# Optimization experiments

Hardware: AMD Instinct MI355X
Metric: run time of the kernel (lower is better)

## Reference

```python
import jax, jax.numpy as jnp
import numpy as np

SEG = 24      # segment_size
NH = 8        # n_heads
THETA = 10000.0


def setup_inputs() -> dict:
    key = jax.random.key(0)
    ks = jax.random.split(key, 6)
    B, T, H, W, D = 8, 96, 32, 32, 64
    in_dim = SEG * D          # 1536
    hid_dim = (SEG // 2) * D  # 768
    n_seg = T // SEG          # 4
    x = jax.random.normal(ks[0], (B, T, H, W, D), dtype=jnp.float32)
    # rotary frequencies: freqs_cis[t, j] = exp(i * t * theta^{-2j/hid_dim})
    inv = 1.0 / (THETA ** (np.arange(0, hid_dim, 2, dtype=np.float32) / hid_dim))
    ang = np.arange(n_seg, dtype=np.float32)[:, None] * inv[None, :]  # (n, hid/2)
    freqs_cos = jnp.asarray(np.cos(ang), dtype=jnp.float32)
    freqs_sin = jnp.asarray(np.sin(ang), dtype=jnp.float32)
    s = 0.02
    Wq = jax.random.normal(ks[1], (in_dim, hid_dim), dtype=jnp.float32) * s
    Wk = jax.random.normal(ks[2], (in_dim, hid_dim), dtype=jnp.float32) * s
    Wv = jax.random.normal(ks[3], (in_dim, hid_dim), dtype=jnp.float32) * s
    Wo = jax.random.normal(ks[4], (hid_dim, in_dim), dtype=jnp.float32) * s
    bo = jnp.zeros((in_dim,), dtype=jnp.float32)
    return {"x": x, "freqs_cos": freqs_cos, "freqs_sin": freqs_sin,
            "Wq": Wq, "Wk": Wk, "Wv": Wv, "Wo": Wo, "bo": bo}


def _rope(q, cos, sin):
    # q: (b, n, hid); pairs (even, odd) rotated by complex multiply
    q2 = q.reshape(*q.shape[:-1], -1, 2)
    qr = q2[..., 0] * cos - q2[..., 1] * sin
    qi = q2[..., 0] * sin + q2[..., 1] * cos
    return jnp.stack([qr, qi], axis=-1).reshape(q.shape)


def reference(x, freqs_cos, freqs_sin, Wq, Wk, Wv, Wo, bo):
    B, T, H, W, D = x.shape
    n = T // SEG
    hid = Wq.shape[1]
    hd = hid // NH
    # (b t h w d) -> ((b h w) n (p d)) ; T divisible by SEG so no padding
    xr = jnp.transpose(x, (0, 2, 3, 1, 4)).reshape(B * H * W, T, D)
    xs = xr.reshape(B * H * W, n, SEG * D)
    q = jnp.einsum('bne,eh->bnh', xs, Wq)
    k = jnp.einsum('bne,eh->bnh', xs, Wk)
    v = jnp.einsum('bne,eh->bnh', xs, Wv)
    cos, sin = freqs_cos[:n][None], freqs_sin[:n][None]  # (1, n, hid/2)
    q = _rope(q, cos, sin)
    k = _rope(k, cos, sin)
    # split heads: b n (h d) -> b h n d
    def heads(t):
        return jnp.transpose(t.reshape(B * H * W, n, NH, hd), (0, 2, 1, 3))
    qh, kh, vh = heads(q), heads(k), heads(v)
    scores = jnp.einsum('bhnd,bhmd->bhnm', qh, kh) / jnp.sqrt(jnp.float32(hd))
    attn = jax.nn.softmax(scores, axis=-1)
    o = jnp.einsum('bhnm,bhmd->bhnd', attn, vh)
    o = jnp.transpose(o, (0, 2, 1, 3)).reshape(B * H * W, n, hid)
    o = jnp.einsum('bnh,he->bne', o, Wo) + bo
    # b n (p d) -> b (n p) d -> (B,T,H,W,D)
    o = o.reshape(B * H * W, T, D)
    o = o.reshape(B, H, W, T, D)
    return jnp.transpose(o, (0, 3, 1, 2, 4))
```

## Files before the change

### kernel.cpp

```cpp
#include <hip/hip_runtime.h>
#include <hip/hip_bf16.h>

using bf16 = __hip_bfloat16;
using short8 = __attribute__((ext_vector_type(8))) short;
using floatx4 = __attribute__((ext_vector_type(4))) float;

#define NSEG 4
#define HID 768
#define INDIM 1536
#define NQKV 2304
#define NHEADS 8
#define HD 96

__device__ inline unsigned short f2b(float v) {
  union { float f; unsigned u; } c; c.f = v;
  unsigned r = c.u + 0x7FFF + ((c.u >> 16) & 1);
  return (unsigned short)(r >> 16);
}
__device__ inline float b2f(unsigned short u) {
  union { unsigned v; float f; } c; c.v = ((unsigned)u) << 16; return c.f;
}

__device__ inline void gload16(const void* g, void* l) {
  __builtin_amdgcn_global_load_lds(
      (const __attribute__((address_space(1))) unsigned int*)g,
      (__attribute__((address_space(3))) unsigned int*)l, 16, 0, 0);
}

#define MEMFENCE asm volatile("" ::: "memory")
#define BARRIER do { MEMFENCE; __builtin_amdgcn_s_barrier(); MEMFENCE; } while (0)

#define PHASE(par, q, LOADB, STAGES, VMW) do {                                 \
    short8 a00 = *(const short8*)(lA + (par)*65536 + (q)*2048);                \
    short8 a01 = *(const short8*)(lA + (par)*65536 + (q)*2048 + 16384);        \
    short8 a10 = *(const short8*)(lA + (par)*65536 + (q)*2048 + 1024);         \
    short8 a11 = *(const short8*)(lA + (par)*65536 + (q)*2048 + 1024 + 16384); \
    if (LOADB) {                                                               \
      _Pragma("unroll")                                                        \
      for (int fn = 0; fn < 4; ++fn) {                                         \
        bfr[fn][0] = *(const short8*)(lB + (par)*65536 + fn*1024);             \
        bfr[fn][1] = *(const short8*)(lB + (par)*65536 + fn*1024 + 16384);     \
      }                                                                        \
    }                                                                          \
    STAGES;                                                                    \
    BARRIER;                                                                   \
    __builtin_amdgcn_s_setprio(1);                                             \
    _Pragma("unroll")                                                          \
    for (int fn = 0; fn < 4; ++fn) {                                           \
      acc[2*(q)][fn]   = __builtin_amdgcn_mfma_f32_16x16x32_bf16(              \
          a00, bfr[fn][0], acc[2*(q)][fn], 0, 0, 0);                           \
      acc[2*(q)][fn]   = __builtin_amdgcn_mfma_f32_16x16x32_bf16(              \
          a01, bfr[fn][1], acc[2*(q)][fn], 0, 0, 0);                           \
      acc[2*(q)+1][fn] = __builtin_amdgcn_mfma_f32_16x16x32_bf16(              \
          a10, bfr[fn][0], acc[2*(q)+1][fn], 0, 0, 0);                         \
      acc[2*(q)+1][fn] = __builtin_amdgcn_mfma_f32_16x16x32_bf16(              \
          a11, bfr[fn][1], acc[2*(q)+1][fn], 0, 0, 0);                         \
    }                                                                          \
    __builtin_amdgcn_s_setprio(0);                                             \
    VMW;                                                                       \
    BARRIER;                                                                   \
  } while (0)

#define VM4 do { asm volatile("s_waitcnt vmcnt(4)" ::: "memory"); } while (0)
#define VM0 do { asm volatile("s_waitcnt vmcnt(0)" ::: "memory"); } while (0)

__global__ __launch_bounds__(256) void transpose_w(
    const float* __restrict__ src, bf16* __restrict__ dst, int K, int C) {
  __shared__ unsigned short tile[32][33];
  const int c0 = blockIdx.x * 32, k0 = blockIdx.y * 32;
  const int tx = threadIdx.x, ty = threadIdx.y;
#pragma unroll
  for (int i = 0; i < 4; ++i)
    tile[ty + 8 * i][tx] = f2b(src[(size_t)(k0 + ty + 8 * i) * C + c0 + tx]);
  __syncthreads();
  unsigned short* d = (unsigned short*)dst;
#pragma unroll
  for (int i = 0; i < 4; ++i)
    d[(size_t)(c0 + ty + 8 * i) * K + k0 + tx] = tile[tx][ty + 8 * i];
}

__global__ __launch_bounds__(256) void transpose_w3(
    const float* __restrict__ s0, const float* __restrict__ s1,
    const float* __restrict__ s2, bf16* __restrict__ dst) {
  __shared__ unsigned short tile[32][33];
  const float* srcs[3] = {s0, s1, s2};
  const float* src = srcs[blockIdx.z];
  bf16* dz = dst + (size_t)blockIdx.z * HID * INDIM;
  const int c0 = blockIdx.x * 32, k0 = blockIdx.y * 32;
  const int tx = threadIdx.x, ty = threadIdx.y;
#pragma unroll
  for (int i = 0; i < 4; ++i)
    tile[ty + 8 * i][tx] = f2b(src[(size_t)(k0 + ty + 8 * i) * HID + c0 + tx]);
  __syncthreads();
  unsigned short* d = (unsigned short*)dz;
#pragma unroll
  for (int i = 0; i < 4; ++i)
    d[(size_t)(c0 + ty + 8 * i) * INDIM + k0 + tx] = tile[tx][ty + 8 * i];
}

__global__ __launch_bounds__(256) void convert_x(
    const float* __restrict__ x, bf16* __restrict__ xb) {
  const size_t i = ((size_t)blockIdx.x * 256 + threadIdx.x) * 8;
  float4 a = *(const float4*)(x + i);
  float4 b = *(const float4*)(x + i + 4);
  union { uint4 u; unsigned short s[8]; } r;
  r.s[0] = f2b(a.x); r.s[1] = f2b(a.y); r.s[2] = f2b(a.z); r.s[3] = f2b(a.w);
  r.s[4] = f2b(b.x); r.s[5] = f2b(b.y); r.s[6] = f2b(b.z); r.s[7] = f2b(b.w);
  *(uint4*)(xb + i) = r.u;
}

__global__ __launch_bounds__(512, 2) void gemm_qkv(
    const bf16* __restrict__ xb, const bf16* __restrict__ wT,
    bf16* __restrict__ qkv) {
  __shared__ __align__(16) char lds[131072];
  const int tid = threadIdx.x;
  const int lane = tid & 63, wave = tid >> 6;
  const int wr = wave >> 2, wc = wave & 3;
  const int l15 = lane & 15, quad = lane >> 4;

  const int lt = (blockIdx.x & 7) * 144 + (blockIdx.x >> 3);
  const int n0 = (lt % 9) * 256;
  const int m0 = (lt / 9) * 256;

  const int srow = wave * 16 + (lane >> 2);
  const int dswz = ((lane & 3) * 8) ^ ((lane & 32) >> 1);
  const bf16* asrc[2];
  const bf16* bsrc[2];
#pragma unroll
  for (int h = 0; h < 2; ++h) {
    const int m = m0 + h * 128 + srow;
    const int r = m >> 2, n = m & 3;
    const int b = r >> 10, hw = r & 1023;
    asrc[h] = xb + ((size_t)((b * 96 + n * 24) * 1024 + hw)) * 64 + dswz;
    bsrc[h] = wT + (size_t)(n0 + h * 128 + srow) * INDIM + dswz;
  }
  char* sdst = lds + wave * 1024;

#define STAGE_QA(kt, h) do {                                   \
    char* d_ = sdst + (((kt) & 1) * 65536) + (h) * 8192;       \
    const bf16* s_ = asrc[h] + (size_t)(kt) * 65536;           \
    gload16(s_, d_);                                           \
    gload16(s_ + 32, d_ + 16384);                              \
  } while (0)
#define STAGE_QB(kt, h) do {                                   \
    char* d_ = sdst + 32768 + (((kt) & 1) * 65536) + (h) * 8192; \
    const bf16* s_ = bsrc[h] + (size_t)(kt) * 64;              \
    gload16(s_, d_);                                           \
    gload16(s_ + 32, d_ + 16384);                              \
  } while (0)

  const int lofs = l15 * 64 + ((quad * 16) ^ ((l15 & 8) << 2));
  const char* lA = lds + wr * 8192 + lofs;
  const char* lB = lds + 32768 + wc * 4096 + lofs;

  floatx4 acc[8][4] = {};
  short8 bfr[4][2];

  STAGE_QB(0, 0); STAGE_QB(0, 1); STAGE_QA(0, 0); STAGE_QA(0, 1);
  STAGE_QB(1, 0); STAGE_QB(1, 1);
  VM4;
  BARRIER;

  const int NKT = 24;
  for (int i = 0; i < 12; ++i) {
    const int a = 2 * i;
    PHASE(0, 0, 1, { STAGE_QA(a + 1, 0); }, {});
    PHASE(0, 1, 0, { STAGE_QA(a + 1, 1); }, {});
    PHASE(0, 2, 0, { if (a + 2 < NKT) STAGE_QB(a + 2, 0); }, {});
    PHASE(0, 3, 0, { if (a + 2 < NKT) STAGE_QB(a + 2, 1); },
          { if (a + 2 < NKT) VM4; else VM0; });
    PHASE(1, 0, 1, { if (a + 2 < NKT) STAGE_QA(a + 2, 0); }, {});
    PHASE(1, 1, 0, { if (a + 2 < NKT) STAGE_QA(a + 2, 1); }, {});
    PHASE(1, 2, 0, { if (a + 3 < NKT) STAGE_QB(a + 3, 0); }, {});
    PHASE(1, 3, 0, { if (a + 3 < NKT) STAGE_QB(a + 3, 1); },
          { if (a + 3 < NKT) VM4; else VM0; });
  }
#undef STAGE_QA
#undef STAGE_QB

#pragma unroll
  for (int fm = 0; fm < 8; ++fm)
#pragma unroll
    for (int fn = 0; fn < 4; ++fn)
#pragma unroll
      for (int reg = 0; reg < 4; ++reg) {
        const int row = m0 + wr * 128 + fm * 16 + quad * 4 + reg;
        const int col = n0 + wc * 64 + fn * 16 + l15;
        qkv[(size_t)row * NQKV + col] = __float2bfloat16(acc[fm][fn][reg]);
      }
}

__global__ __launch_bounds__(256) void attn_kernel(
    const bf16* __restrict__ qkv, const float* __restrict__ fcos,
    const float* __restrict__ fsin, bf16* __restrict__ obuf) {
  const int wave = threadIdx.x >> 6, lane = threadIdx.x & 63;
  const int r = blockIdx.x * 4 + wave;
  const int c0 = lane * 12;
  const int j0 = lane * 6;
  const bf16* base = qkv + (size_t)r * (NSEG * NQKV) + c0;

  float q[NSEG][12], k[NSEG][12];
#pragma unroll
  for (int n = 0; n < NSEG; ++n) {
    const bf16* row = base + (size_t)n * NQKV;
    union { uint2 u[3]; unsigned short s[12]; } Q, K;
#pragma unroll
    for (int t = 0; t < 3; ++t) {
      Q.u[t] = *(const uint2*)(row + 4 * t);
      K.u[t] = *(const uint2*)(row + HID + 4 * t);
    }
    const float* cp = fcos + n * (HID / 2) + j0;
    const float* sp = fsin + n * (HID / 2) + j0;
#pragma unroll
    for (int t = 0; t < 6; ++t) {
      const float cc = cp[t], ss = sp[t];
      const float a = b2f(Q.s[2 * t]), b = b2f(Q.s[2 * t + 1]);
      q[n][2 * t] = a * cc - b * ss;
      q[n][2 * t + 1] = a * ss + b * cc;
      const float e = b2f(K.s[2 * t]), f = b2f(K.s[2 * t + 1]);
      k[n][2 * t] = e * cc - f * ss;
      k[n][2 * t + 1] = e * ss + f * cc;
    }
  }

  float P[NSEG][NSEG];
#pragma unroll
  for (int n = 0; n < NSEG; ++n)
#pragma unroll
    for (int m = 0; m < NSEG; ++m) {
      float s = 0.f;
#pragma unroll
      for (int t = 0; t < 12; ++t) s += q[n][t] * k[m][t];
      s += __shfl_xor(s, 1, 64);
      s += __shfl_xor(s, 2, 64);
      s += __shfl_xor(s, 4, 64);
      P[n][m] = s * 0.10206207261596575f;
    }
#pragma unroll
  for (int n = 0; n < NSEG; ++n) {
    const float mx = fmaxf(fmaxf(P[n][0], P[n][1]), fmaxf(P[n][2], P[n][3]));
    float sum = 0.f;
#pragma unroll
    for (int m = 0; m < NSEG; ++m) {
      P[n][m] = __expf(P[n][m] - mx);
      sum += P[n][m];
    }
    const float inv = 1.f / sum;
#pragma unroll
    for (int m = 0; m < NSEG; ++m) P[n][m] *= inv;
  }

  float v[NSEG][12];
#pragma unroll
  for (int n = 0; n < NSEG; ++n) {
    union { uint2 u[3]; unsigned short s[12]; } V;
#pragma unroll
    for (int t = 0; t < 3; ++t)
      V.u[t] = *(const uint2*)(base + (size_t)n * NQKV + 2 * HID + 4 * t);
#pragma unroll
    for (int t = 0; t < 12; ++t) v[n][t] = b2f(V.s[t]);
  }
  bf16* orow = obuf + (size_t)r * (NSEG * HID) + c0;
#pragma unroll
  for (int n = 0; n < NSEG; ++n) {
    union { uint2 u[3]; unsigned w[6]; } O;
#pragma unroll
    for (int t = 0; t < 6; ++t) {
      float o0 = 0.f, o1 = 0.f;
#pragma unroll
      for (int m = 0; m < NSEG; ++m) {
        o0 += P[n][m] * v[m][2 * t];
        o1 += P[n][m] * v[m][2 * t + 1];
      }
      O.w[t] = (unsigned)f2b(o0) | ((unsigned)f2b(o1) << 16);
    }
#pragma unroll
    for (int t = 0; t < 3; ++t)
      *(uint2*)(orow + (size_t)n * HID + 4 * t) = O.u[t];
  }
}

__global__ __launch_bounds__(512, 2) void gemm_out(
    const bf16* __restrict__ Ao, const bf16* __restrict__ wT,
    const float* __restrict__ bo, float* __restrict__ out) {
  __shared__ __align__(16) char lds[131072];
  const int tid = threadIdx.x;
  const int lane = tid & 63, wave = tid >> 6;
  const int wr = wave >> 2, wc = wave & 3;
  const int l15 = lane & 15, quad = lane >> 4;

  const int lt = (blockIdx.x & 7) * 96 + (blockIdx.x >> 3);
  const int n0 = (lt % 6) * 256;
  const int m0 = (lt / 6) * 256;

  const int srow = wave * 16 + (lane >> 2);
  const int dswz = ((lane & 3) * 8) ^ ((lane & 32) >> 1);
  const bf16* asrc[2];
  const bf16* bsrc[2];
#pragma unroll
  for (int h = 0; h < 2; ++h) {
    asrc[h] = Ao + (size_t)(m0 + h * 128 + srow) * HID + dswz;
    bsrc[h] = wT + (size_t)(n0 + h * 128 + srow) * HID + dswz;
  }
  char* sdst = lds + wave * 1024;

#define STAGE_OA(kt, h) do {                                   \
    char* d_ = sdst + (((kt) & 1) * 65536) + (h) * 8192;       \
    const bf16* s_ = asrc[h] + (size_t)(kt) * 64;              \
    gload16(s_, d_);                                           \
    gload16(s_ + 32, d_ + 16384);                              \
  } while (0)
#define STAGE_OB(kt, h) do {                                   \
    char* d_ = sdst + 32768 + (((kt) & 1) * 65536) + (h) * 8192; \
    const bf16* s_ = bsrc[h] + (size_t)(kt) * 64;              \
    gload16(s_, d_);                                           \
    gload16(s_ + 32, d_ + 16384);                              \
  } while (0)

  const int lofs = l15 * 64 + ((quad * 16) ^ ((l15 & 8) << 2));
  const char* lA = lds + wr * 8192 + lofs;
  const char* lB = lds + 32768 + wc * 4096 + lofs;

  floatx4 acc[8][4] = {};
  short8 bfr[4][2];

  STAGE_OB(0, 0); STAGE_OB(0, 1); STAGE_OA(0, 0); STAGE_OA(0, 1);
  STAGE_OB(1, 0); STAGE_OB(1, 1);
  VM4;
  BARRIER;

  const int NKT = 12;
  for (int i = 0; i < 6; ++i) {
    const int a = 2 * i;
    PHASE(0, 0, 1, { STAGE_OA(a + 1, 0); }, {});
    PHASE(0, 1, 0, { STAGE_OA(a + 1, 1); }, {});
    PHASE(0, 2, 0, { if (a + 2 < NKT) STAGE_OB(a + 2, 0); }, {});
    PHASE(0, 3, 0, { if (a + 2 < NKT) STAGE_OB(a + 2, 1); },
          { if (a + 2 < NKT) VM4; else VM0; });
    PHASE(1, 0, 1, { if (a + 2 < NKT) STAGE_OA(a + 2, 0); }, {});
    PHASE(1, 1, 0, { if (a + 2 < NKT) STAGE_OA(a + 2, 1); }, {});
    PHASE(1, 2, 0, { if (a + 3 < NKT) STAGE_OB(a + 3, 0); }, {});
    PHASE(1, 3, 0, { if (a + 3 < NKT) STAGE_OB(a + 3, 1); },
          { if (a + 3 < NKT) VM4; else VM0; });
  }
#undef STAGE_OA
#undef STAGE_OB

#pragma unroll
  for (int fm = 0; fm < 8; ++fm)
#pragma unroll
    for (int fn = 0; fn < 4; ++fn)
#pragma unroll
      for (int reg = 0; reg < 4; ++reg) {
        const int row = m0 + wr * 128 + fm * 16 + quad * 4 + reg;
        const int col = n0 + wc * 64 + fn * 16 + l15;
        const float v = acc[fm][fn][reg] + bo[col];
        const int r = row >> 2, n = row & 3;
        const int b = r >> 10, hw = r & 1023;
        const int p = col >> 6, d = col & 63;
        const size_t dst =
            ((size_t)((b * 96 + n * 24 + p) * 1024 + hw)) * 64 + d;
        out[dst] = v;
      }
}

extern "C" void kernel_launch(void* const* d_in, const int* in_sizes, int n_in,
                              void* d_out, int out_size, void* d_ws,
                              size_t ws_size, hipStream_t stream) {
  const float* x = (const float*)d_in[0];
  const float* fcos = (const float*)d_in[1];
  const float* fsin = (const float*)d_in[2];
  const float* Wq = (const float*)d_in[3];
  const float* Wk = (const float*)d_in[4];
  const float* Wv = (const float*)d_in[5];
  const float* Wo = (const float*)d_in[6];
  const float* bo = (const float*)d_in[7];
  float* out = (float*)d_out;

  char* ws = (char*)d_ws;
  bf16* wqkvT = (bf16*)ws;
  bf16* woT = (bf16*)(ws + 7077888);
  bf16* qkv = (bf16*)(ws + 9437184);
  bf16* obuf = (bf16*)(ws + 160432128);
  bf16* xb = (bf16*)d_out;

  dim3 tb(32, 8);
  transpose_w3<<<dim3(24, 48, 3), tb, 0, stream>>>(Wq, Wk, Wv, wqkvT);
  transpose_w<<<dim3(48, 24), tb, 0, stream>>>(Wo, woT, HID, INDIM);

  convert_x<<<24576, 256, 0, stream>>>(x, xb);
  gemm_qkv<<<1152, 512, 0, stream>>>(xb, wqkvT, qkv);
  attn_kernel<<<2048, 256, 0, stream>>>(qkv, fcos, fsin, obuf);
  gemm_out<<<768, 512, 0, stream>>>(obuf, woT, bo, out);
}
```

Baseline: 684.3 us.

## Merge weight transposes into one launch, widen convert_x, restructure attention Q loading

Combines the two weight-transpose kernels into one launch over a 48x48x4 grid, with an early exit for out-of-range tiles, to save a launch. convert_x now handles 16 elements per thread with half as many blocks. The attention kernel loads and rotates Q one segment at a time inside the score loop instead of keeping all Q in registers, and adds an occupancy hint of 4 blocks via launch bounds, to lower register pressure. The merged grid launches idle blocks for the smaller Wo shape.

```diff
diff --git a/kernel.cpp b/kernel.cpp
--- a/kernel.cpp
+++ b/kernel.cpp
@@ -64,49 +64,48 @@
 #define VM4 do { asm volatile("s_waitcnt vmcnt(4)" ::: "memory"); } while (0)
 #define VM0 do { asm volatile("s_waitcnt vmcnt(0)" ::: "memory"); } while (0)
 
-__global__ __launch_bounds__(256) void transpose_w(
-    const float* __restrict__ src, bf16* __restrict__ dst, int K, int C) {
+__global__ __launch_bounds__(256) void transpose_all(
+    const float* __restrict__ Wq, const float* __restrict__ Wk,
+    const float* __restrict__ Wv, const float* __restrict__ Wo,
+    bf16* __restrict__ wqkvT, bf16* __restrict__ woT) {
   __shared__ unsigned short tile[32][33];
+  const int z = blockIdx.z;
+  const float* src;
+  unsigned short* dst;
+  int K, C;
+  if (z < 3) {
+    src = (z == 0) ? Wq : (z == 1) ? Wk : Wv;
+    dst = (unsigned short*)(wqkvT + (size_t)z * HID * INDIM);
+    K = INDIM; C = HID;
+  } else {
+    src = Wo;
+    dst = (unsigned short*)woT;
+    K = HID; C = INDIM;
+  }
   const int c0 = blockIdx.x * 32, k0 = blockIdx.y * 32;
+  if (c0 >= C || k0 >= K) return;
   const int tx = threadIdx.x, ty = threadIdx.y;
 #pragma unroll
   for (int i = 0; i < 4; ++i)
     tile[ty + 8 * i][tx] = f2b(src[(size_t)(k0 + ty + 8 * i) * C + c0 + tx]);
   __syncthreads();
-  unsigned short* d = (unsigned short*)dst;
 #pragma unroll
   for (int i = 0; i < 4; ++i)
-    d[(size_t)(c0 + ty + 8 * i) * K + k0 + tx] = tile[tx][ty + 8 * i];
-}
-
-__global__ __launch_bounds__(256) void transpose_w3(
-    const float* __restrict__ s0, const float* __restrict__ s1,
-    const float* __restrict__ s2, bf16* __restrict__ dst) {
-  __shared__ unsigned short tile[32][33];
-  const float* srcs[3] = {s0, s1, s2};
-  const float* src = srcs[blockIdx.z];
-  bf16* dz = dst + (size_t)blockIdx.z * HID * INDIM;
-  const int c0 = blockIdx.x * 32, k0 = blockIdx.y * 32;
-  const int tx = threadIdx.x, ty = threadIdx.y;
-#pragma unroll
-  for (int i = 0; i < 4; ++i)
-    tile[ty + 8 * i][tx] = f2b(src[(size_t)(k0 + ty + 8 * i) * HID + c0 + tx]);
-  __syncthreads();
-  unsigned short* d = (unsigned short*)dz;
-#pragma unroll
-  for (int i = 0; i < 4; ++i)
-    d[(size_t)(c0 + ty + 8 * i) * INDIM + k0 + tx] = tile[tx][ty + 8 * i];
+    dst[(size_t)(c0 + ty + 8 * i) * K + k0 + tx] = tile[tx][ty + 8 * i];
 }
 
 __global__ __launch_bounds__(256) void convert_x(
     const float* __restrict__ x, bf16* __restrict__ xb) {
-  const size_t i = ((size_t)blockIdx.x * 256 + threadIdx.x) * 8;
-  float4 a = *(const float4*)(x + i);
-  float4 b = *(const float4*)(x + i + 4);
-  union { uint4 u; unsigned short s[8]; } r;
-  r.s[0] = f2b(a.x); r.s[1] = f2b(a.y); r.s[2] = f2b(a.z); r.s[3] = f2b(a.w);
-  r.s[4] = f2b(b.x); r.s[5] = f2b(b.y); r.s[6] = f2b(b.z); r.s[7] = f2b(b.w);
-  *(uint4*)(xb + i) = r.u;
+  const size_t i = ((size_t)blockIdx.x * 256 + threadIdx.x) * 16;
+#pragma unroll
+  for (int h = 0; h < 2; ++h) {
+    float4 a = *(const float4*)(x + i + 8 * h);
+    float4 b = *(const float4*)(x + i + 8 * h + 4);
+    union { uint4 u; unsigned short s[8]; } r;
+    r.s[0] = f2b(a.x); r.s[1] = f2b(a.y); r.s[2] = f2b(a.z); r.s[3] = f2b(a.w);
+    r.s[4] = f2b(b.x); r.s[5] = f2b(b.y); r.s[6] = f2b(b.z); r.s[7] = f2b(b.w);
+    *(uint4*)(xb + i + 8 * h) = r.u;
+  }
 }
 
 __global__ __launch_bounds__(512, 2) void gemm_qkv(
@@ -190,7 +189,7 @@
       }
 }
 
-__global__ __launch_bounds__(256) void attn_kernel(
+__global__ __launch_bounds__(256, 4) void attn_kernel(
     const bf16* __restrict__ qkv, const float* __restrict__ fcos,
     const float* __restrict__ fsin, bf16* __restrict__ obuf) {
   const int wave = threadIdx.x >> 6, lane = threadIdx.x & 63;
@@ -199,24 +198,18 @@
   const int j0 = lane * 6;
   const bf16* base = qkv + (size_t)r * (NSEG * NQKV) + c0;
 
-  float q[NSEG][12], k[NSEG][12];
+  float k[NSEG][12];
 #pragma unroll
   for (int n = 0; n < NSEG; ++n) {
-    const bf16* row = base + (size_t)n * NQKV;
-    union { uint2 u[3]; unsigned short s[12]; } Q, K;
-#pragma unroll
-    for (int t = 0; t < 3; ++t) {
-      Q.u[t] = *(const uint2*)(row + 4 * t);
-      K.u[t] = *(const uint2*)(row + HID + 4 * t);
-    }
+    union { uint2 u[3]; unsigned short s[12]; } K;
+#pragma unroll
+    for (int t = 0; t < 3; ++t)
+      K.u[t] = *(const uint2*)(base + (size_t)n * NQKV + HID + 4 * t);
     const float* cp = fcos + n * (HID / 2) + j0;
     const float* sp = fsin + n * (HID / 2) + j0;
 #pragma unroll
     for (int t = 0; t < 6; ++t) {
       const float cc = cp[t], ss = sp[t];
-      const float a = b2f(Q.s[2 * t]), b = b2f(Q.s[2 * t + 1]);
-      q[n][2 * t] = a * cc - b * ss;
-      q[n][2 * t + 1] = a * ss + b * cc;
       const float e = b2f(K.s[2 * t]), f = b2f(K.s[2 * t + 1]);
       k[n][2 * t] = e * cc - f * ss;
       k[n][2 * t + 1] = e * ss + f * cc;
@@ -225,17 +218,33 @@
 
   float P[NSEG][NSEG];
 #pragma unroll
-  for (int n = 0; n < NSEG; ++n)
+  for (int n = 0; n < NSEG; ++n) {
+    union { uint2 u[3]; unsigned short s[12]; } Q;
+#pragma unroll
+    for (int t = 0; t < 3; ++t)
+      Q.u[t] = *(const uint2*)(base + (size_t)n * NQKV + 4 * t);
+    const float* cp = fcos + n * (HID / 2) + j0;
+    const float* sp = fsin + n * (HID / 2) + j0;
+    float q[12];
+#pragma unroll
+    for (int t = 0; t < 6; ++t) {
+      const float cc = cp[t], ss = sp[t];
+      const float a = b2f(Q.s[2 * t]), b = b2f(Q.s[2 * t + 1]);
+      q[2 * t] = a * cc - b * ss;
+      q[2 * t + 1] = a * ss + b * cc;
+    }
 #pragma unroll
     for (int m = 0; m < NSEG; ++m) {
       float s = 0.f;
 #pragma unroll
-      for (int t = 0; t < 12; ++t) s += q[n][t] * k[m][t];
+      for (int t = 0; t < 12; ++t) s += q[t] * k[m][t];
       s += __shfl_xor(s, 1, 64);
       s += __shfl_xor(s, 2, 64);
       s += __shfl_xor(s, 4, 64);
       P[n][m] = s * 0.10206207261596575f;
     }
+  }
+
 #pragma unroll
   for (int n = 0; n < NSEG; ++n) {
     const float mx = fmaxf(fmaxf(P[n][0], P[n][1]), fmaxf(P[n][2], P[n][3]));
@@ -384,11 +393,9 @@
   bf16* obuf = (bf16*)(ws + 160432128);
   bf16* xb = (bf16*)d_out;
 
-  dim3 tb(32, 8);
-  transpose_w3<<<dim3(24, 48, 3), tb, 0, stream>>>(Wq, Wk, Wv, wqkvT);
-  transpose_w<<<dim3(48, 24), tb, 0, stream>>>(Wo, woT, HID, INDIM);
-
-  convert_x<<<24576, 256, 0, stream>>>(x, xb);
+  transpose_all<<<dim3(48, 48, 4), dim3(32, 8), 0, stream>>>(
+      Wq, Wk, Wv, Wo, wqkvT, woT);
+  convert_x<<<12288, 256, 0, stream>>>(x, xb);
   gemm_qkv<<<1152, 512, 0, stream>>>(xb, wqkvT, qkv);
   attn_kernel<<<2048, 256, 0, stream>>>(qkv, fcos, fsin, obuf);
   gemm_out<<<768, 512, 0, stream>>>(obuf, woT, bo, out);
```

After: 695.5 us. No clear change (+1.6%).
